# Performance work log

Hardware: AMD Instinct MI355X
Metric: run time of the kernel (lower is better)

The kernel has to match this reference:

```python
import jax, jax.numpy as jnp
import numpy as np
import math

NH = 8      # n_heads
EPS = 1e-5  # LayerNorm eps (torch default)

def _pe(S, D):
    # Sin/cos positional encoding, faithful to PositionalEncoder
    pos = jnp.arange(S, dtype=jnp.float32)[:, None]
    div = jnp.exp(jnp.arange(0, D, 2, dtype=jnp.float32) * (-math.log(10000.0) / D))
    ang = pos * div  # (S, D/2)
    pe = jnp.zeros((S, D), jnp.float32)
    pe = pe.at[:, 0::2].set(jnp.sin(ang)).at[:, 1::2].set(jnp.cos(ang))
    return pe

def _ln(x, g, b):
    m = x.mean(-1, keepdims=True)
    v = ((x - m) ** 2).mean(-1, keepdims=True)
    return (x - m) / jnp.sqrt(v + EPS) * g + b

def setup_inputs() -> dict:
    key = jax.random.key(0)
    ks = jax.random.split(key, 6)
    S, H, W, D, dff = 512, 4, 4, 512, 2048
    x = jax.random.normal(ks[0], (S, H, W, D), jnp.float32)
    s = 1.0 / math.sqrt(D)
    Wq = jax.random.normal(ks[1], (D, D), jnp.float32) * s      # w_qs (used for q, k, v in sincos path)
    Wfc = jax.random.normal(ks[2], (D, D), jnp.float32) * s     # fc (no bias)
    W1 = jax.random.normal(ks[3], (dff, D), jnp.float32) * s    # ffn.w1
    b1 = jnp.zeros((dff,), jnp.float32)
    W2 = jax.random.normal(ks[4], (D, dff), jnp.float32) * (1.0 / math.sqrt(dff))  # ffn.w2
    b2 = jnp.zeros((D,), jnp.float32)
    g1 = jnp.ones((D,), jnp.float32); be1 = jnp.zeros((D,), jnp.float32)
    g2 = jnp.ones((D,), jnp.float32); be2 = jnp.zeros((D,), jnp.float32)
    return dict(x=x, Wq=Wq, Wfc=Wfc, W1=W1, b1=b1, W2=W2, b2=b2,
                g1=g1, be1=be1, g2=g2, be2=be2)

def reference(x, Wq, Wfc, W1, b1, W2, b2, g1, be1, g2, be2):
    S, H, Wd, D = x.shape
    depth = D // NH
    # sincos path: ALL of q,k,v use w_qs (source bug) and q==k==v since inputs are identical
    q = x @ Wq.T + _pe(S, D)[:, None, None, :]               # (S,H,W,D)
    # torch .view: raw memory reinterpretation (S,H,W,D) -> (H,W,S,NH,depth), then transpose(2,3)
    q5 = jnp.swapaxes(q.reshape(H, Wd, S, NH, depth), 2, 3)  # (H,W,NH,S,depth)
    k_t = jnp.swapaxes(q5, 3, 4)                             # (H,W,NH,depth,S)
    scale = 1.0 / math.sqrt(depth)
    # 'hwink,hwijm->hwinm': k and j are summed INDEPENDENTLY (rank-1 outer product of sums)
    bmm_qk = jnp.einsum('hwink,hwijm->hwinm', q5 * scale, k_t)   # (H,W,NH,S,S)
    qk = jax.nn.softmax(bmm_qk, axis=-1)
    qk = jnp.einsum('hwink,hwijm->hwinm', qk, k_t)               # second context pass
    attn_weights = jax.nn.softmax(qk, axis=-1)
    out = jnp.einsum('hwijk,hwikn->hwijn', attn_weights, q5)     # v == q5; (H,W,NH,S,depth)
    attn_out = out.reshape(S, H, Wd, NH * depth) @ Wfc.T         # raw reshape back, then fc
    o1 = _ln(x + attn_out, g1, be1)
    ffn = jax.nn.relu(o1 @ W1.T + b1) @ W2.T + b2
    return _ln(o1 + ffn, g2, be2)
```

## Files before the change

kernel.cpp:

```cpp
#include <hip/hip_runtime.h>
#include <hip/hip_bf16.h>
#include <math.h>


typedef short short8 __attribute__((ext_vector_type(8)));
typedef float f32x4 __attribute__((ext_vector_type(4)));

#define LN10K_OVER_256 0.03597789207803197f

__device__ __forceinline__ void gload16(const short* g, short* l) {
  __builtin_amdgcn_global_load_lds(
      (const __attribute__((address_space(1))) void*)g,
      (__attribute__((address_space(3))) void*)l, 16, 0, 0);
}

#define BAR() do { asm volatile("" ::: "memory"); \
                   __builtin_amdgcn_s_barrier();  \
                   asm volatile("" ::: "memory"); } while (0)

__device__ __forceinline__ void xcd_swizzle(int& bx, int& by) {
  int gx = gridDim.x, nwg = gx * gridDim.y;
  int o = blockIdx.x + blockIdx.y * gx;
  int wid = (o & 7) * (nwg >> 3) + (o >> 3);
  bx = wid % gx;
  by = wid / gx;
}

__device__ __forceinline__ short8 ldsfrag(const short* opbuf, int R, int fq) {
  int sr = R >> 1;
  int sp = (((R & 1) << 2) | fq) ^ (sr & 7);
  return *(const short8*)(opbuf + sr * 64 + sp * 8);
}

template<bool DOSTAGE, int WAITK>
__device__ __forceinline__ void tile_step(
    short* ldsb, int cur, int nx, int tt,
    const short* Ag0, const short* Ag1, const short* Bg0, const short* Bg1,
    int w, int fr, int fq, int wm, int wn, f32x4 (&acc)[8][4]) {
  const short* Abuf = ldsb + cur * 16384;
  const short* Bbuf = Abuf + 8192;
  short8 af[4], bfr[4];
#pragma unroll
  for (int m = 0; m < 4; ++m) af[m] = ldsfrag(Abuf, wm + m * 16 + fr, fq);
#pragma unroll
  for (int n = 0; n < 4; ++n) bfr[n] = ldsfrag(Bbuf, wn + n * 16 + fr, fq);
  if (DOSTAGE) {
    int kb = (tt + 2) * 32;
    gload16(Ag0 + kb, ldsb + nx * 16384 + w * 512);
    gload16(Ag1 + kb, ldsb + nx * 16384 + 4096 + w * 512);
  }
  BAR();
  __builtin_amdgcn_s_setprio(1);
#pragma unroll
  for (int m = 0; m < 4; ++m)
#pragma unroll
    for (int n = 0; n < 4; ++n)
      acc[m][n] = __builtin_amdgcn_mfma_f32_16x16x32_bf16(af[m], bfr[n],
                                                          acc[m][n], 0, 0, 0);
  __builtin_amdgcn_s_setprio(0);
  BAR();
#pragma unroll
  for (int m = 0; m < 4; ++m) af[m] = ldsfrag(Abuf, wm + 64 + m * 16 + fr, fq);
  if (DOSTAGE) {
    int kb = (tt + 2) * 32;
    gload16(Bg0 + kb, ldsb + nx * 16384 + 8192 + w * 512);
    gload16(Bg1 + kb, ldsb + nx * 16384 + 8192 + 4096 + w * 512);
  }
  BAR();
  __builtin_amdgcn_s_setprio(1);
#pragma unroll
  for (int m = 0; m < 4; ++m)
#pragma unroll
    for (int n = 0; n < 4; ++n)
      acc[4 + m][n] = __builtin_amdgcn_mfma_f32_16x16x32_bf16(af[m], bfr[n],
                                                              acc[4 + m][n], 0, 0, 0);
  __builtin_amdgcn_s_setprio(0);
  if (WAITK == 4) asm volatile("s_waitcnt vmcnt(4)" ::: "memory");
  else if (WAITK == 0) asm volatile("s_waitcnt vmcnt(0)" ::: "memory");
  BAR();
}

template<int MODE, int NT>
__global__ __launch_bounds__(512) void gemm256(
    const short* __restrict__ A, const short* __restrict__ B,
    const float* __restrict__ bias, short* __restrict__ C0,
    int ldC, int ldA, int ldB) {
  __shared__ short lds[3 * 2 * 8192];
  const int t = threadIdx.x;
  const int w = t >> 6, l = t & 63;
  const int fr = l & 15, fq = l >> 4;
  const int wm = (w >> 2) * 128;
  const int wn = (w & 3) * 64;
  int bx, by;
  xcd_swizzle(bx, by);
  const int m0 = by * 256, n0 = bx * 256;

  const int scont = (t & 7) ^ ((t >> 3) & 7);
  const int Rbase = ((t >> 3) << 1) | (scont >> 2);
  const int cg = (scont & 3) << 3;
  const short* Ag0 = A + (size_t)(m0 + Rbase) * ldA + cg;
  const short* Ag1 = Ag0 + (size_t)128 * ldA;
  const short* Bg0 = B + (size_t)(n0 + Rbase) * ldB + cg;
  const short* Bg1 = Bg0 + (size_t)128 * ldB;
  short* ldsb = &lds[0];

  gload16(Ag0, ldsb + w * 512);
  gload16(Ag1, ldsb + 4096 + w * 512);
  gload16(Bg0, ldsb + 8192 + w * 512);
  gload16(Bg1, ldsb + 8192 + 4096 + w * 512);
  gload16(Ag0 + 32, ldsb + 16384 + w * 512);
  gload16(Ag1 + 32, ldsb + 16384 + 4096 + w * 512);
  gload16(Bg0 + 32, ldsb + 16384 + 8192 + w * 512);
  gload16(Bg1 + 32, ldsb + 16384 + 8192 + 4096 + w * 512);
  asm volatile("s_waitcnt vmcnt(4)" ::: "memory");
  BAR();

  f32x4 acc[8][4] = {};
  int cur = 0;
#pragma unroll 1
  for (int tt = 0; tt < NT - 2; ++tt) {
    int nx = cur + 2; if (nx >= 3) nx -= 3;
    tile_step<true, 4>(ldsb, cur, nx, tt, Ag0, Ag1, Bg0, Bg1,
                       w, fr, fq, wm, wn, acc);
    if (++cur == 3) cur = 0;
  }
  tile_step<false, 0>(ldsb, cur, 0, NT - 2, Ag0, Ag1, Bg0, Bg1,
                      w, fr, fq, wm, wn, acc);
  { int c2 = cur + 1; if (c2 >= 3) c2 -= 3;
    tile_step<false, -1>(ldsb, c2, 0, NT - 1, Ag0, Ag1, Bg0, Bg1,
                         w, fr, fq, wm, wn, acc); }

  float bv[4];
#pragma unroll
  for (int n = 0; n < 4; ++n) bv[n] = bias[n0 + wn + n * 16 + fr];
#pragma unroll
  for (int mm = 0; mm < 8; ++mm) {
#pragma unroll
    for (int n = 0; n < 4; ++n) {
      int col = n0 + wn + n * 16 + fr;
#pragma unroll
      for (int j = 0; j < 4; ++j) {
        int row = m0 + wm + mm * 16 + fq * 4 + j;
        float v = fmaxf(acc[mm][n][j] + bv[n], 0.f);
        __hip_bfloat16 hb = __float2bfloat16(v);
        C0[(size_t)row * ldC + col] = *(short*)&hb;
      }
    }
  }
}

template<bool DOSTAGE, int WAITK>
__device__ __forceinline__ void tile_step128(
    short* ldsb, int cur, int nx, int tt,
    const short* Ag0, const short* Ag1, const short* Bg0, const short* Bg1,
    int w, int fr, int fq, int wm, int wn, f32x4 (&acc)[4][4]) {
  const short* Abuf = ldsb + cur * 8192;
  const short* Bbuf = Abuf + 4096;
  short8 af[4], bfr[4];
#pragma unroll
  for (int m = 0; m < 4; ++m) af[m] = ldsfrag(Abuf, wm + m * 16 + fr, fq);
#pragma unroll
  for (int n = 0; n < 4; ++n) bfr[n] = ldsfrag(Bbuf, wn + n * 16 + fr, fq);
  if (DOSTAGE) {
    int kb = (tt + 2) * 32;
    gload16(Ag0 + kb, ldsb + nx * 8192 + w * 512);
    gload16(Ag1 + kb, ldsb + nx * 8192 + 2048 + w * 512);
    gload16(Bg0 + kb, ldsb + nx * 8192 + 4096 + w * 512);
    gload16(Bg1 + kb, ldsb + nx * 8192 + 6144 + w * 512);
  }
  BAR();
  __builtin_amdgcn_s_setprio(1);
#pragma unroll
  for (int m = 0; m < 4; ++m)
#pragma unroll
    for (int n = 0; n < 4; ++n)
      acc[m][n] = __builtin_amdgcn_mfma_f32_16x16x32_bf16(af[m], bfr[n],
                                                          acc[m][n], 0, 0, 0);
  __builtin_amdgcn_s_setprio(0);
  if (WAITK == 4) asm volatile("s_waitcnt vmcnt(4)" ::: "memory");
  else if (WAITK == 0) asm volatile("s_waitcnt vmcnt(0)" ::: "memory");
  BAR();
}

template<int MODE, int NT>
__global__ __launch_bounds__(256) void gemm128(
    const short* __restrict__ A, const short* __restrict__ B,
    const float* __restrict__ bias, short* __restrict__ C,
    int ldC, int ldA, int ldB) {
  __shared__ short lds[3 * 8192];
  const int t = threadIdx.x;
  const int w = t >> 6, l = t & 63;
  const int fr = l & 15, fq = l >> 4;
  const int wm = (w >> 1) * 64;
  const int wn = (w & 1) * 64;
  int bx, by;
  xcd_swizzle(bx, by);
  const int m0 = by * 128, n0 = bx * 128;

  const int scont = (t & 7) ^ ((t >> 3) & 7);
  const int Rbase = ((t >> 3) << 1) | (scont >> 2);
  const int cg = (scont & 3) << 3;
  const short* Ag0 = A + (size_t)(m0 + Rbase) * ldA + cg;
  const short* Ag1 = Ag0 + (size_t)64 * ldA;
  const short* Bg0 = B + (size_t)(n0 + Rbase) * ldB + cg;
  const short* Bg1 = Bg0 + (size_t)64 * ldB;
  short* ldsb = &lds[0];

  gload16(Ag0, ldsb + w * 512);
  gload16(Ag1, ldsb + 2048 + w * 512);
  gload16(Bg0, ldsb + 4096 + w * 512);
  gload16(Bg1, ldsb + 6144 + w * 512);
  gload16(Ag0 + 32, ldsb + 8192 + w * 512);
  gload16(Ag1 + 32, ldsb + 8192 + 2048 + w * 512);
  gload16(Bg0 + 32, ldsb + 8192 + 4096 + w * 512);
  gload16(Bg1 + 32, ldsb + 8192 + 6144 + w * 512);
  asm volatile("s_waitcnt vmcnt(4)" ::: "memory");
  BAR();

  f32x4 acc[4][4] = {};
  int cur = 0;
#pragma unroll 1
  for (int tt = 0; tt < NT - 2; ++tt) {
    int nx = cur + 2; if (nx >= 3) nx -= 3;
    tile_step128<true, 4>(ldsb, cur, nx, tt, Ag0, Ag1, Bg0, Bg1,
                          w, fr, fq, wm, wn, acc);
    if (++cur == 3) cur = 0;
  }
  tile_step128<false, 0>(ldsb, cur, 0, NT - 2, Ag0, Ag1, Bg0, Bg1,
                         w, fr, fq, wm, wn, acc);
  { int c2 = cur + 1; if (c2 >= 3) c2 -= 3;
    tile_step128<false, -1>(ldsb, c2, 0, NT - 1, Ag0, Ag1, Bg0, Bg1,
                            w, fr, fq, wm, wn, acc); }

  float bv[4];
  if (MODE == 2) {
#pragma unroll
    for (int n = 0; n < 4; ++n) bv[n] = bias[n0 + wn + n * 16 + fr];
  }
#pragma unroll
  for (int mm = 0; mm < 4; ++mm) {
    const float* per = nullptr;
    if (MODE == 0) {
      int s = (m0 + wm + mm * 16) >> 4;
      per = bias + (size_t)s * 512;
    }
#pragma unroll
    for (int n = 0; n < 4; ++n) {
      int col = n0 + wn + n * 16 + fr;
      float pv = (MODE == 0) ? per[col] : bv[n];
#pragma unroll
      for (int j = 0; j < 4; ++j) {
        int row = m0 + wm + mm * 16 + fq * 4 + j;
        float v = acc[mm][n][j] + pv;
        __hip_bfloat16 hb = __float2bfloat16(v);
        C[(size_t)row * ldC + col] = *(short*)&hb;
      }
    }
  }
}

__device__ __forceinline__ void cvt8(const float* in, short* out, int i) {
  const float4* p = (const float4*)(in + (size_t)i * 8);
  float4 a = p[0], b = p[1];
  union { __hip_bfloat16 h[8]; short8 s; } u;
  u.h[0] = __float2bfloat16(a.x); u.h[1] = __float2bfloat16(a.y);
  u.h[2] = __float2bfloat16(a.z); u.h[3] = __float2bfloat16(a.w);
  u.h[4] = __float2bfloat16(b.x); u.h[5] = __float2bfloat16(b.y);
  u.h[6] = __float2bfloat16(b.z); u.h[7] = __float2bfloat16(b.w);
  *(short8*)(out + (size_t)i * 8) = u.s;
}

__global__ __launch_bounds__(256) void prep(
    const float* __restrict__ x, const float* __restrict__ W1,
    const float* __restrict__ W2, const float* __restrict__ Wq,
    const float* __restrict__ Wfc,
    short* __restrict__ xb, short* __restrict__ W1b,
    short* __restrict__ W2b, short* __restrict__ Wqb,
    float* __restrict__ wsum, float* __restrict__ pe) {
  int b = blockIdx.x, t = threadIdx.x;
  if (b < 2048) {
    cvt8(x, xb, b * 256 + t);
  } else if (b < 2560) {
    cvt8(W1, W1b, (b - 2048) * 256 + t);
  } else if (b < 3072) {
    cvt8(W2, W2b, (b - 2560) * 256 + t);
  } else if (b < 3200) {
    cvt8(Wq, Wqb, (b - 3072) * 256 + t);
  } else if (b < 3328) {
    int idx = (b - 3200) * 256 + t;
    int n = idx >> 6, d = idx & 63;
    float s = 0.f;
#pragma unroll
    for (int j = 0; j < 8; ++j) s += Wfc[(size_t)n * 512 + j * 64 + d];
    wsum[idx] = s;
  } else {
    int idx = (b - 3328) * 256 + t;
    int s = idx >> 9, c = idx & 511;
    float f = expf(-(float)(c >> 1) * LN10K_OVER_256);
    float ang = (float)s * f;
    pe[idx] = (c & 1) ? cosf(ang) : sinf(ang);
  }
}

__global__ __launch_bounds__(256) void attn_g(
    const short* __restrict__ qb, const float* __restrict__ x,
    const float* __restrict__ wsum, const float* __restrict__ g1,
    const float* __restrict__ be1, short* __restrict__ o1b) {
  int g = blockIdx.x;
  int hw = g >> 3, i = g & 7;
  int t = threadIdx.x;
  __shared__ short sl[512 * 72];
  __shared__ float a_[512];
  __shared__ float adist_[512];
  __shared__ float pctx[4][64];
  __shared__ float gb[1024];
  __shared__ float redA[4], redB[4], redMS[2];
  __shared__ float ctxs[64];

  gb[t] = g1[t]; gb[t + 256] = g1[t + 256];
  gb[512 + t] = be1[t]; gb[768 + t] = be1[t + 256];

  {
    const short* qsrc = qb + ((size_t)hw * 512) * 512 + i * 64;
    int chunk = t & 7, jr0 = t >> 3;
#pragma unroll
    for (int rep = 0; rep < 16; ++rep) {
      int j = jr0 + rep * 32;
      *(short8*)&sl[j * 72 + chunk * 8] =
          *(const short8*)(qsrc + (size_t)j * 512 + chunk * 8);
    }
  }
  __syncthreads();

  float r0 = 0.f, r1 = 0.f;
#pragma unroll
  for (int c = 0; c < 8; ++c) {
    union { short8 s8; short e[8]; } u0, u1;
    u0.s8 = *(const short8*)&sl[t * 72 + c * 8];
    u1.s8 = *(const short8*)&sl[(t + 256) * 72 + c * 8];
#pragma unroll
    for (int u = 0; u < 8; ++u) {
      r0 += __bfloat162float(*(__hip_bfloat16*)&u0.e[u]);
      r1 += __bfloat162float(*(__hip_bfloat16*)&u1.e[u]);
    }
  }
  float m = fmaxf(r0, r1);
  for (int off = 32; off; off >>= 1) m = fmaxf(m, __shfl_down(m, off));
  int wid = t >> 6, lane = t & 63;
  if (lane == 0) redA[wid] = m;
  __syncthreads();
  if (t == 0) redMS[0] = fmaxf(fmaxf(redA[0], redA[1]), fmaxf(redA[2], redA[3]));
  __syncthreads();
  float M = redMS[0];
  float e0 = expf(r0 - M), e1 = expf(r1 - M);
  float s = e0 + e1;
  for (int off = 32; off; off >>= 1) s += __shfl_down(s, off);
  if (lane == 0) redB[wid] = s;
  __syncthreads();
  if (t == 0) redMS[1] = redB[0] + redB[1] + redB[2] + redB[3];
  __syncthreads();
  float inv = 1.f / redMS[1];
  a_[t] = e0 * inv;
  a_[t + 256] = e1 * inv;
  __syncthreads();

  {
    int d = t & 63, seg = t >> 6;
    float acc = 0.f;
    for (int mm = seg * 128; mm < seg * 128 + 128; ++mm)
      acc += a_[mm] * __bfloat162float(*(__hip_bfloat16*)&sl[mm * 72 + d]);
    pctx[seg][d] = acc;
  }
  __syncthreads();
  if (t < 64) ctxs[t] = pctx[0][t] + pctx[1][t] + pctx[2][t] + pctx[3][t];
  __syncthreads();

  for (int n = t; n < 512; n += 256) {
    const float4* wr = (const float4*)(wsum + (size_t)n * 64);
    float sa = 0.f;
#pragma unroll
    for (int db = 0; db < 16; ++db) {
      float4 wv = wr[db];
      float4 cv = *(const float4*)&ctxs[db * 4];
      sa += cv.x * wv.x + cv.y * wv.y + cv.z * wv.z + cv.w * wv.w;
    }
    adist_[n] = sa;
  }
  __syncthreads();

  const float4* x4 = (const float4*)x;
  int w = t >> 6;
#pragma unroll 1
  for (int u = 0; u < 16; ++u) {
    int j = i * 64 + w * 16 + u;
    size_t R = (size_t)hw * 512 + j;
    float4 xv0 = x4[R * 128 + lane * 2];
    float4 xv1 = x4[R * 128 + lane * 2 + 1];
    float4 a0 = *(const float4*)&adist_[lane * 8];
    float4 a1 = *(const float4*)&adist_[lane * 8 + 4];
    float v[8] = {xv0.x + a0.x, xv0.y + a0.y, xv0.z + a0.z, xv0.w + a0.w,
                  xv1.x + a1.x, xv1.y + a1.y, xv1.z + a1.z, xv1.w + a1.w};
    float sm_ = 0.f, sq = 0.f;
#pragma unroll
    for (int q = 0; q < 8; ++q) { sm_ += v[q]; sq += v[q] * v[q]; }
    for (int off = 32; off; off >>= 1) {
      sm_ += __shfl_xor(sm_, off);
      sq += __shfl_xor(sq, off);
    }
    float mean = sm_ * (1.f / 512.f);
    float var = sq * (1.f / 512.f) - mean * mean;
    float rinv = rsqrtf(var + 1e-5f);
    union { __hip_bfloat16 h[8]; short8 s8; } ub;
#pragma unroll
    for (int q = 0; q < 8; ++q) {
      int c = lane * 8 + q;
      ub.h[q] = __float2bfloat16((v[q] - mean) * rinv * gb[c] + gb[512 + c]);
    }
    *(short8*)&o1b[R * 512 + lane * 8] = ub.s8;
  }
}

__global__ __launch_bounds__(256) void ln2_fused(
    const short* __restrict__ o1b, const short* __restrict__ f2,
    const float* __restrict__ gamma, const float* __restrict__ beta,
    float* __restrict__ Out) {
  int t = threadIdx.x;
  int wv = t >> 6, lane = t & 63;
  size_t r = (size_t)blockIdx.x * 4 + wv;
  size_t base = r * 512 + lane * 8;
  union { short8 s8; short e[8]; } uo, uf;
  uo.s8 = *(const short8*)&o1b[base];
  uf.s8 = *(const short8*)&f2[base];
  float v[8];
  float s = 0.f, sq = 0.f;
#pragma unroll
  for (int k = 0; k < 8; ++k) {
    v[k] = __bfloat162float(*(__hip_bfloat16*)&uo.e[k]) +
           __bfloat162float(*(__hip_bfloat16*)&uf.e[k]);
    s += v[k];
    sq += v[k] * v[k];
  }
  for (int off = 32; off; off >>= 1) {
    s += __shfl_xor(s, off);
    sq += __shfl_xor(sq, off);
  }
  float mean = s * (1.f / 512.f);
  float var = sq * (1.f / 512.f) - mean * mean;
  float inv = rsqrtf(var + 1e-5f);
  int c0 = lane * 8;
  float4 g0 = *(const float4*)&gamma[c0];
  float4 g1v = *(const float4*)&gamma[c0 + 4];
  float4 b0 = *(const float4*)&beta[c0];
  float4 b1v = *(const float4*)&beta[c0 + 4];
  float4 o0, o1v;
  o0.x = (v[0] - mean) * inv * g0.x + b0.x;
  o0.y = (v[1] - mean) * inv * g0.y + b0.y;
  o0.z = (v[2] - mean) * inv * g0.z + b0.z;
  o0.w = (v[3] - mean) * inv * g0.w + b0.w;
  o1v.x = (v[4] - mean) * inv * g1v.x + b1v.x;
  o1v.y = (v[5] - mean) * inv * g1v.y + b1v.y;
  o1v.z = (v[6] - mean) * inv * g1v.z + b1v.z;
  o1v.w = (v[7] - mean) * inv * g1v.w + b1v.w;
  *(float4*)&Out[base] = o0;
  *(float4*)&Out[base + 4] = o1v;
}

extern "C" void kernel_launch(void* const* d_in, const int* in_sizes, int n_in,
                              void* d_out, int out_size, void* d_ws, size_t ws_size,
                              hipStream_t stream) {
  const float* x   = (const float*)d_in[0];
  const float* Wq  = (const float*)d_in[1];
  const float* Wfc = (const float*)d_in[2];
  const float* W1  = (const float*)d_in[3];
  const float* b1  = (const float*)d_in[4];
  const float* W2  = (const float*)d_in[5];
  const float* b2  = (const float*)d_in[6];
  const float* g1  = (const float*)d_in[7];
  const float* be1 = (const float*)d_in[8];
  const float* g2  = (const float*)d_in[9];
  const float* be2 = (const float*)d_in[10];
  float* out = (float*)d_out;

  char* ws = (char*)d_ws;
  short* h1b  = (short*)(ws);
  short* f2b  = (short*)(ws + (32u << 20));
  short* o1b  = (short*)(ws + (40u << 20));
  short* W1b  = (short*)(ws + (48u << 20));
  short* W2b  = (short*)(ws + (50u << 20));
  short* Wqb  = (short*)(ws + (52u << 20));
  short* xb   = (short*)(ws + (53u << 20));
  short* qb   = (short*)(ws + (61u << 20));
  float* wsum = (float*)(ws + (69u << 20));
  float* pe   = (float*)(ws + (69u << 20) + (128u << 10));

  prep<<<4352, 256, 0, stream>>>(x, W1, W2, Wq, Wfc, xb, W1b, W2b, Wqb, wsum, pe);
  gemm128<0, 16><<<dim3(4, 64), 256, 0, stream>>>(
      xb, Wqb, pe, qb, 512, 512, 512);
  attn_g<<<128, 256, 0, stream>>>(qb, x, wsum, g1, be1, o1b);
  gemm256<1, 16><<<dim3(8, 32), 512, 0, stream>>>(
      o1b, W1b, b1, h1b, 2048, 512, 512);
  gemm128<2, 64><<<dim3(4, 64), 256, 0, stream>>>(
      h1b, W2b, b2, f2b, 512, 2048, 2048);
  ln2_fused<<<2048, 256, 0, stream>>>(o1b, f2b, g2, be2, out);
}
```

Before: 94.66 us.

## Add K=64 128x128 GEMM for FFN down-projection and merge gemm256 barrier phases

Adds a new gemm128x64 kernel that stages 64-wide K tiles (twice the old depth) with an XOR-swizzled 64-element LDS row layout. Each stage does two MFMA sub-steps, so the W2 GEMM takes 32 iterations instead of 64 and pays half as many barriers and waits. The change also restructures gemm256's tile_step: it loads all eight A fragments up front and issues A and B global loads together, which removes one barrier pair per step at the cost of more registers. It also drops the hoisted bias registers in gemm128 in favour of per-column bias loads.

```diff
diff --git a/kernel.cpp b/kernel.cpp
--- a/kernel.cpp
+++ b/kernel.cpp
@@ -30,6 +30,10 @@
   int sr = R >> 1;
   int sp = (((R & 1) << 2) | fq) ^ (sr & 7);
   return *(const short8*)(opbuf + sr * 64 + sp * 8);
+}
+
+__device__ __forceinline__ short8 ldsfrag64(const short* opbuf, int R, int s) {
+  return *(const short8*)(opbuf + R * 64 + ((s ^ (R & 7)) * 8));
 }
 
 template<bool DOSTAGE, int WAITK>
@@ -39,15 +43,18 @@
     int w, int fr, int fq, int wm, int wn, f32x4 (&acc)[8][4]) {
   const short* Abuf = ldsb + cur * 16384;
   const short* Bbuf = Abuf + 8192;
-  short8 af[4], bfr[4];
-#pragma unroll
-  for (int m = 0; m < 4; ++m) af[m] = ldsfrag(Abuf, wm + m * 16 + fr, fq);
+  short8 af[8], bfr[4];
+#pragma unroll
+  for (int m = 0; m < 8; ++m)
+    af[m] = ldsfrag(Abuf, wm + (m >> 2) * 64 + (m & 3) * 16 + fr, fq);
 #pragma unroll
   for (int n = 0; n < 4; ++n) bfr[n] = ldsfrag(Bbuf, wn + n * 16 + fr, fq);
   if (DOSTAGE) {
     int kb = (tt + 2) * 32;
     gload16(Ag0 + kb, ldsb + nx * 16384 + w * 512);
     gload16(Ag1 + kb, ldsb + nx * 16384 + 4096 + w * 512);
+    gload16(Bg0 + kb, ldsb + nx * 16384 + 8192 + w * 512);
+    gload16(Bg1 + kb, ldsb + nx * 16384 + 8192 + 4096 + w * 512);
   }
   BAR();
   __builtin_amdgcn_s_setprio(1);
@@ -57,22 +64,11 @@
     for (int n = 0; n < 4; ++n)
       acc[m][n] = __builtin_amdgcn_mfma_f32_16x16x32_bf16(af[m], bfr[n],
                                                           acc[m][n], 0, 0, 0);
-  __builtin_amdgcn_s_setprio(0);
-  BAR();
-#pragma unroll
-  for (int m = 0; m < 4; ++m) af[m] = ldsfrag(Abuf, wm + 64 + m * 16 + fr, fq);
-  if (DOSTAGE) {
-    int kb = (tt + 2) * 32;
-    gload16(Bg0 + kb, ldsb + nx * 16384 + 8192 + w * 512);
-    gload16(Bg1 + kb, ldsb + nx * 16384 + 8192 + 4096 + w * 512);
-  }
-  BAR();
-  __builtin_amdgcn_s_setprio(1);
 #pragma unroll
   for (int m = 0; m < 4; ++m)
 #pragma unroll
     for (int n = 0; n < 4; ++n)
-      acc[4 + m][n] = __builtin_amdgcn_mfma_f32_16x16x32_bf16(af[m], bfr[n],
+      acc[4 + m][n] = __builtin_amdgcn_mfma_f32_16x16x32_bf16(af[4 + m], bfr[n],
                                                               acc[4 + m][n], 0, 0, 0);
   __builtin_amdgcn_s_setprio(0);
   if (WAITK == 4) asm volatile("s_waitcnt vmcnt(4)" ::: "memory");
@@ -232,11 +228,6 @@
     tile_step128<false, -1>(ldsb, c2, 0, NT - 1, Ag0, Ag1, Bg0, Bg1,
                             w, fr, fq, wm, wn, acc); }
 
-  float bv[4];
-  if (MODE == 2) {
-#pragma unroll
-    for (int n = 0; n < 4; ++n) bv[n] = bias[n0 + wn + n * 16 + fr];
-  }
 #pragma unroll
   for (int mm = 0; mm < 4; ++mm) {
     const float* per = nullptr;
@@ -247,11 +238,126 @@
 #pragma unroll
     for (int n = 0; n < 4; ++n) {
       int col = n0 + wn + n * 16 + fr;
-      float pv = (MODE == 0) ? per[col] : bv[n];
+      float pv = (MODE == 0) ? per[col] : bias[col];
 #pragma unroll
       for (int j = 0; j < 4; ++j) {
         int row = m0 + wm + mm * 16 + fq * 4 + j;
         float v = acc[mm][n][j] + pv;
+        __hip_bfloat16 hb = __float2bfloat16(v);
+        C[(size_t)row * ldC + col] = *(short*)&hb;
+      }
+    }
+  }
+}
+
+template<bool DOSTAGE, int WAITK>
+__device__ __forceinline__ void tile_step64(
+    short* ldsb, int cur, int nx, int tt,
+    const short* Ag, const short* Bg, int ldA, int ldB,
+    int w, int fr, int fq, int wm, int wn, f32x4 (&acc)[4][4]) {
+  const short* Abuf = ldsb + cur * 16384;
+  const short* Bbuf = Abuf + 8192;
+  short8 af[4], bfr[4];
+#pragma unroll
+  for (int m = 0; m < 4; ++m) af[m] = ldsfrag64(Abuf, wm + m * 16 + fr, fq);
+#pragma unroll
+  for (int n = 0; n < 4; ++n) bfr[n] = ldsfrag64(Bbuf, wn + n * 16 + fr, fq);
+  if (DOSTAGE) {
+    int kb = (tt + 2) * 64;
+    short* dst = ldsb + nx * 16384;
+#pragma unroll
+    for (int i = 0; i < 4; ++i) {
+      gload16(Ag + kb + (size_t)(i * 8) * ldA, dst + (w * 4 + i) * 512);
+      gload16(Bg + kb + (size_t)(i * 8) * ldB, dst + 8192 + (w * 4 + i) * 512);
+    }
+  }
+  BAR();
+  __builtin_amdgcn_s_setprio(1);
+#pragma unroll
+  for (int m = 0; m < 4; ++m)
+#pragma unroll
+    for (int n = 0; n < 4; ++n)
+      acc[m][n] = __builtin_amdgcn_mfma_f32_16x16x32_bf16(af[m], bfr[n],
+                                                          acc[m][n], 0, 0, 0);
+  __builtin_amdgcn_s_setprio(0);
+#pragma unroll
+  for (int m = 0; m < 4; ++m) af[m] = ldsfrag64(Abuf, wm + m * 16 + fr, 4 + fq);
+#pragma unroll
+  for (int n = 0; n < 4; ++n) bfr[n] = ldsfrag64(Bbuf, wn + n * 16 + fr, 4 + fq);
+  __builtin_amdgcn_s_setprio(1);
+#pragma unroll
+  for (int m = 0; m < 4; ++m)
+#pragma unroll
+    for (int n = 0; n < 4; ++n)
+      acc[m][n] = __builtin_amdgcn_mfma_f32_16x16x32_bf16(af[m], bfr[n],
+                                                          acc[m][n], 0, 0, 0);
+  __builtin_amdgcn_s_setprio(0);
+  if (WAITK == 8) asm volatile("s_waitcnt vmcnt(8)" ::: "memory");
+  else if (WAITK == 0) asm volatile("s_waitcnt vmcnt(0)" ::: "memory");
+  BAR();
+}
+
+template<int NT>
+__global__ __launch_bounds__(256) void gemm128x64(
+    const short* __restrict__ A, const short* __restrict__ B,
+    const float* __restrict__ bias, short* __restrict__ C,
+    int ldC, int ldA, int ldB) {
+  __shared__ short lds[3 * 16384];
+  const int t = threadIdx.x;
+  const int w = t >> 6, l = t & 63;
+  const int fr = l & 15, fq = l >> 4;
+  const int wm = (w >> 1) * 64;
+  const int wn = (w & 1) * 64;
+  int bx, by;
+  xcd_swizzle(bx, by);
+  const int m0 = by * 128, n0 = bx * 128;
+
+  const int rb = l >> 3;
+  const int cgp = ((l & 7) ^ rb) * 8;
+  const short* Ag = A + (size_t)(m0 + w * 32 + rb) * ldA + cgp;
+  const short* Bg = B + (size_t)(n0 + w * 32 + rb) * ldB + cgp;
+  short* ldsb = &lds[0];
+
+#pragma unroll
+  for (int tb = 0; tb < 2; ++tb) {
+    short* dst = ldsb + tb * 16384;
+    int kb = tb * 64;
+#pragma unroll
+    for (int i = 0; i < 4; ++i) {
+      gload16(Ag + kb + (size_t)(i * 8) * ldA, dst + (w * 4 + i) * 512);
+      gload16(Bg + kb + (size_t)(i * 8) * ldB, dst + 8192 + (w * 4 + i) * 512);
+    }
+  }
+  asm volatile("s_waitcnt vmcnt(8)" ::: "memory");
+  BAR();
+
+  f32x4 acc[4][4] = {};
+  int cur = 0;
+#pragma unroll 1
+  for (int tt = 0; tt < NT - 2; ++tt) {
+    int nx = cur + 2; if (nx >= 3) nx -= 3;
+    tile_step64<true, 8>(ldsb, cur, nx, tt, Ag, Bg, ldA, ldB,
+                         w, fr, fq, wm, wn, acc);
+    if (++cur == 3) cur = 0;
+  }
+  tile_step64<false, 0>(ldsb, cur, 0, NT - 2, Ag, Bg, ldA, ldB,
+                        w, fr, fq, wm, wn, acc);
+  { int c2 = cur + 1; if (c2 >= 3) c2 -= 3;
+    tile_step64<false, -1>(ldsb, c2, 0, NT - 1, Ag, Bg, ldA, ldB,
+                           w, fr, fq, wm, wn, acc); }
+
+  float bv[4];
+#pragma unroll
+  for (int n = 0; n < 4; ++n) bv[n] = bias[n0 + wn + n * 16 + fr];
+#pragma unroll
+  for (int mm = 0; mm < 4; ++mm) {
+#pragma unroll
+    for (int n = 0; n < 4; ++n) {
+      int col = n0 + wn + n * 16 + fr;
+#pragma unroll
+      for (int j = 0; j < 4; ++j) {
+        int row = m0 + wm + mm * 16 + fq * 4 + j;
+        float v = acc[mm][n][j] + bv[n];
         __hip_bfloat16 hb = __float2bfloat16(v);
         C[(size_t)row * ldC + col] = *(short*)&hb;
       }
@@ -499,7 +605,7 @@
   attn_g<<<128, 256, 0, stream>>>(qb, x, wsum, g1, be1, o1b);
   gemm256<1, 16><<<dim3(8, 32), 512, 0, stream>>>(
       o1b, W1b, b1, h1b, 2048, 512, 512);
-  gemm128<2, 64><<<dim3(4, 64), 256, 0, stream>>>(
+  gemm128x64<32><<<dim3(4, 64), 256, 0, stream>>>(
       h1b, W2b, b2, f2b, 512, 2048, 2048);
   ln2_fused<<<2048, 256, 0, stream>>>(o1b, f2b, g2, be2, out);
 }
```

Result: no change. 93.59 us (-1.1%).

## Use 8-wave 128x128 GEMM blocks and merge 256-tile half-steps into one barrier phase

Applied to the files above, without the earlier changes.

The 128x128 GEMM now runs with 512 threads (8 waves), each computing a 32x64 sub-tile. Each thread issues half as many global-to-LDS loads per k-step, and the vmcnt wait shrinks to match. In the 256x256 kernel, all eight A fragments are loaded up front and both A and B stages are issued together. This removes the middle barrier pair so 32 MFMAs run back to back. The trade is more waves competing for LDS bandwidth and more registers per thread in the 256 kernel, in exchange for more latency hiding and fewer barriers.

```diff
diff --git a/kernel.cpp b/kernel.cpp
--- a/kernel.cpp
+++ b/kernel.cpp
@@ -39,15 +39,18 @@
     int w, int fr, int fq, int wm, int wn, f32x4 (&acc)[8][4]) {
   const short* Abuf = ldsb + cur * 16384;
   const short* Bbuf = Abuf + 8192;
-  short8 af[4], bfr[4];
-#pragma unroll
-  for (int m = 0; m < 4; ++m) af[m] = ldsfrag(Abuf, wm + m * 16 + fr, fq);
+  short8 af[8], bfr[4];
+#pragma unroll
+  for (int m = 0; m < 8; ++m)
+    af[m] = ldsfrag(Abuf, wm + (m >> 2) * 64 + (m & 3) * 16 + fr, fq);
 #pragma unroll
   for (int n = 0; n < 4; ++n) bfr[n] = ldsfrag(Bbuf, wn + n * 16 + fr, fq);
   if (DOSTAGE) {
     int kb = (tt + 2) * 32;
     gload16(Ag0 + kb, ldsb + nx * 16384 + w * 512);
     gload16(Ag1 + kb, ldsb + nx * 16384 + 4096 + w * 512);
+    gload16(Bg0 + kb, ldsb + nx * 16384 + 8192 + w * 512);
+    gload16(Bg1 + kb, ldsb + nx * 16384 + 8192 + 4096 + w * 512);
   }
   BAR();
   __builtin_amdgcn_s_setprio(1);
@@ -57,22 +60,11 @@
     for (int n = 0; n < 4; ++n)
       acc[m][n] = __builtin_amdgcn_mfma_f32_16x16x32_bf16(af[m], bfr[n],
                                                           acc[m][n], 0, 0, 0);
-  __builtin_amdgcn_s_setprio(0);
-  BAR();
-#pragma unroll
-  for (int m = 0; m < 4; ++m) af[m] = ldsfrag(Abuf, wm + 64 + m * 16 + fr, fq);
-  if (DOSTAGE) {
-    int kb = (tt + 2) * 32;
-    gload16(Bg0 + kb, ldsb + nx * 16384 + 8192 + w * 512);
-    gload16(Bg1 + kb, ldsb + nx * 16384 + 8192 + 4096 + w * 512);
-  }
-  BAR();
-  __builtin_amdgcn_s_setprio(1);
 #pragma unroll
   for (int m = 0; m < 4; ++m)
 #pragma unroll
     for (int n = 0; n < 4; ++n)
-      acc[4 + m][n] = __builtin_amdgcn_mfma_f32_16x16x32_bf16(af[m], bfr[n],
+      acc[4 + m][n] = __builtin_amdgcn_mfma_f32_16x16x32_bf16(af[4 + m], bfr[n],
                                                               acc[4 + m][n], 0, 0, 0);
   __builtin_amdgcn_s_setprio(0);
   if (WAITK == 4) asm volatile("s_waitcnt vmcnt(4)" ::: "memory");
@@ -150,40 +142,39 @@
 }
 
 template<bool DOSTAGE, int WAITK>
-__device__ __forceinline__ void tile_step128(
+__device__ __forceinline__ void tile_step128w8(
     short* ldsb, int cur, int nx, int tt,
-    const short* Ag0, const short* Ag1, const short* Bg0, const short* Bg1,
-    int w, int fr, int fq, int wm, int wn, f32x4 (&acc)[4][4]) {
+    const short* Ag, const short* Bg,
+    int w, int fr, int fq, int wm, int wn, f32x4 (&acc)[2][4]) {
   const short* Abuf = ldsb + cur * 8192;
   const short* Bbuf = Abuf + 4096;
-  short8 af[4], bfr[4];
-#pragma unroll
-  for (int m = 0; m < 4; ++m) af[m] = ldsfrag(Abuf, wm + m * 16 + fr, fq);
+  short8 af[2], bfr[4];
+#pragma unroll
+  for (int m = 0; m < 2; ++m) af[m] = ldsfrag(Abuf, wm + m * 16 + fr, fq);
 #pragma unroll
   for (int n = 0; n < 4; ++n) bfr[n] = ldsfrag(Bbuf, wn + n * 16 + fr, fq);
   if (DOSTAGE) {
     int kb = (tt + 2) * 32;
-    gload16(Ag0 + kb, ldsb + nx * 8192 + w * 512);
-    gload16(Ag1 + kb, ldsb + nx * 8192 + 2048 + w * 512);
-    gload16(Bg0 + kb, ldsb + nx * 8192 + 4096 + w * 512);
-    gload16(Bg1 + kb, ldsb + nx * 8192 + 6144 + w * 512);
+    short* dst = ldsb + nx * 8192;
+    gload16(Ag + kb, dst + w * 512);
+    gload16(Bg + kb, dst + 4096 + w * 512);
   }
   BAR();
   __builtin_amdgcn_s_setprio(1);
 #pragma unroll
-  for (int m = 0; m < 4; ++m)
+  for (int m = 0; m < 2; ++m)
 #pragma unroll
     for (int n = 0; n < 4; ++n)
       acc[m][n] = __builtin_amdgcn_mfma_f32_16x16x32_bf16(af[m], bfr[n],
                                                           acc[m][n], 0, 0, 0);
   __builtin_amdgcn_s_setprio(0);
-  if (WAITK == 4) asm volatile("s_waitcnt vmcnt(4)" ::: "memory");
+  if (WAITK == 2) asm volatile("s_waitcnt vmcnt(2)" ::: "memory");
   else if (WAITK == 0) asm volatile("s_waitcnt vmcnt(0)" ::: "memory");
   BAR();
 }
 
 template<int MODE, int NT>
-__global__ __launch_bounds__(256) void gemm128(
+__global__ __launch_bounds__(512) void gemm128w8(
     const short* __restrict__ A, const short* __restrict__ B,
     const float* __restrict__ bias, short* __restrict__ C,
     int ldC, int ldA, int ldB) {
@@ -191,7 +182,7 @@
   const int t = threadIdx.x;
   const int w = t >> 6, l = t & 63;
   const int fr = l & 15, fq = l >> 4;
-  const int wm = (w >> 1) * 64;
+  const int wm = (w >> 1) * 32;
   const int wn = (w & 1) * 64;
   int bx, by;
   xcd_swizzle(bx, by);
@@ -200,45 +191,34 @@
   const int scont = (t & 7) ^ ((t >> 3) & 7);
   const int Rbase = ((t >> 3) << 1) | (scont >> 2);
   const int cg = (scont & 3) << 3;
-  const short* Ag0 = A + (size_t)(m0 + Rbase) * ldA + cg;
-  const short* Ag1 = Ag0 + (size_t)64 * ldA;
-  const short* Bg0 = B + (size_t)(n0 + Rbase) * ldB + cg;
-  const short* Bg1 = Bg0 + (size_t)64 * ldB;
+  const short* Ag = A + (size_t)(m0 + Rbase) * ldA + cg;
+  const short* Bg = B + (size_t)(n0 + Rbase) * ldB + cg;
   short* ldsb = &lds[0];
 
-  gload16(Ag0, ldsb + w * 512);
-  gload16(Ag1, ldsb + 2048 + w * 512);
-  gload16(Bg0, ldsb + 4096 + w * 512);
-  gload16(Bg1, ldsb + 6144 + w * 512);
-  gload16(Ag0 + 32, ldsb + 8192 + w * 512);
-  gload16(Ag1 + 32, ldsb + 8192 + 2048 + w * 512);
-  gload16(Bg0 + 32, ldsb + 8192 + 4096 + w * 512);
-  gload16(Bg1 + 32, ldsb + 8192 + 6144 + w * 512);
-  asm volatile("s_waitcnt vmcnt(4)" ::: "memory");
-  BAR();
-
-  f32x4 acc[4][4] = {};
+  gload16(Ag, ldsb + w * 512);
+  gload16(Bg, ldsb + 4096 + w * 512);
+  gload16(Ag + 32, ldsb + 8192 + w * 512);
+  gload16(Bg + 32, ldsb + 8192 + 4096 + w * 512);
+  asm volatile("s_waitcnt vmcnt(2)" ::: "memory");
+  BAR();
+
+  f32x4 acc[2][4] = {};
   int cur = 0;
 #pragma unroll 1
   for (int tt = 0; tt < NT - 2; ++tt) {
     int nx = cur + 2; if (nx >= 3) nx -= 3;
-    tile_step128<true, 4>(ldsb, cur, nx, tt, Ag0, Ag1, Bg0, Bg1,
-                          w, fr, fq, wm, wn, acc);
+    tile_step128w8<true, 2>(ldsb, cur, nx, tt, Ag, Bg,
+                            w, fr, fq, wm, wn, acc);
     if (++cur == 3) cur = 0;
   }
-  tile_step128<false, 0>(ldsb, cur, 0, NT - 2, Ag0, Ag1, Bg0, Bg1,
-                         w, fr, fq, wm, wn, acc);
+  tile_step128w8<false, 0>(ldsb, cur, 0, NT - 2, Ag, Bg,
+                           w, fr, fq, wm, wn, acc);
   { int c2 = cur + 1; if (c2 >= 3) c2 -= 3;
-    tile_step128<false, -1>(ldsb, c2, 0, NT - 1, Ag0, Ag1, Bg0, Bg1,
-                            w, fr, fq, wm, wn, acc); }
-
-  float bv[4];
-  if (MODE == 2) {
-#pragma unroll
-    for (int n = 0; n < 4; ++n) bv[n] = bias[n0 + wn + n * 16 + fr];
-  }
-#pragma unroll
-  for (int mm = 0; mm < 4; ++mm) {
+    tile_step128w8<false, -1>(ldsb, c2, 0, NT - 1, Ag, Bg,
+                              w, fr, fq, wm, wn, acc); }
+
+#pragma unroll
+  for (int mm = 0; mm < 2; ++mm) {
     const float* per = nullptr;
     if (MODE == 0) {
       int s = (m0 + wm + mm * 16) >> 4;
@@ -247,7 +227,7 @@
 #pragma unroll
     for (int n = 0; n < 4; ++n) {
       int col = n0 + wn + n * 16 + fr;
-      float pv = (MODE == 0) ? per[col] : bv[n];
+      float pv = (MODE == 0) ? per[col] : bias[col];
 #pragma unroll
       for (int j = 0; j < 4; ++j) {
         int row = m0 + wm + mm * 16 + fq * 4 + j;
@@ -494,12 +474,12 @@
   float* pe   = (float*)(ws + (69u << 20) + (128u << 10));
 
   prep<<<4352, 256, 0, stream>>>(x, W1, W2, Wq, Wfc, xb, W1b, W2b, Wqb, wsum, pe);
-  gemm128<0, 16><<<dim3(4, 64), 256, 0, stream>>>(
+  gemm128w8<0, 16><<<dim3(4, 64), 512, 0, stream>>>(
       xb, Wqb, pe, qb, 512, 512, 512);
   attn_g<<<128, 256, 0, stream>>>(qb, x, wsum, g1, be1, o1b);
   gemm256<1, 16><<<dim3(8, 32), 512, 0, stream>>>(
       o1b, W1b, b1, h1b, 2048, 512, 512);
-  gemm128<2, 64><<<dim3(4, 64), 256, 0, stream>>>(
+  gemm128w8<2, 64><<<dim3(4, 64), 512, 0, stream>>>(
       h1b, W2b, b2, f2b, 512, 2048, 2048);
   ln2_fused<<<2048, 256, 0, stream>>>(o1b, f2b, g2, be2, out);
 }
```

Result: no change. 95.87 us (+1.3%).
